# Performance work log

Measured on AMD Instinct MI355X. Metric: run time of the kernel, lower is better.

## Reference

```python
import jax, jax.numpy as jnp
import numpy as np

B, V, D = 2048, 3129, 768  # batch, answer vocab, BERT embed dim


def setup_inputs() -> dict:
    key = jax.random.key(0)
    k1, k2, k3, k4 = jax.random.split(key, 4)
    prediction = jax.random.normal(k1, (B, V), dtype=jnp.float32)
    # sparse multi-label soft scores: ~10 nonzero answers per row (VQA-style)
    soft = jax.random.uniform(k2, (B, V), dtype=jnp.float32)
    keep = jax.random.uniform(k3, (B, V)) < 0.003
    label = jnp.where(keep, soft, 0.0)
    Embedding = jax.random.normal(k4, (V, D), dtype=jnp.float32)
    return {"prediction": prediction, "label": label, "Embedding": Embedding}


def reference(prediction, label, Embedding):
    V_ = Embedding.shape[0]
    # cosine-style normalization of the Gram matrix (row norms of sim itself,
    # exactly as in the torch code)
    sim = Embedding @ Embedding.T                              # [V, V]
    n = jnp.sqrt((sim ** 2).sum(1, keepdims=True))             # [V, 1]
    sim = sim / (n @ n.T + 1e-8)
    sim = jnp.where(jnp.eye(V_, dtype=bool), -2.0, sim)        # mask diagonal
    mapping = jnp.argmax(sim, axis=1)                          # [V] int

    # vectorized replacement of the per-batch/per-nonzero python loop:
    # semantic_a[i, mapping[g]] = label[i, g] for every nonzero label[i, g].
    # entries with label==0 are routed to out-of-bounds index V and dropped.
    Bn = label.shape[0]
    idx = jnp.where(label != 0, mapping[None, :], V_)          # [B, V]
    rows = jnp.arange(Bn)[:, None]                             # [B, 1]
    semantic_a = jnp.zeros_like(label).at[rows, idx].set(label, mode="drop")

    # BCE-with-logits, mean reduction, scaled by labels.size(1)
    bce = jnp.logaddexp(0.0, prediction) - prediction * semantic_a
    return jnp.mean(bce) * V_
```

## Files before the change

kernel.cpp:

```cpp
#include <hip/hip_runtime.h>
#include <hip/hip_bf16.h>

#define VN 3129
#define DN 768
#define BN 2048
#define NT 3200
#define NB64 50
#define NTRI64 1275
#define NBLK_LOGEXP 512
#define NBLK_COMPACT 512
#define GRID_MEGA2 (NTRI64 + NBLK_LOGEXP + NBLK_COMPACT)

typedef __attribute__((ext_vector_type(8))) short bf16x8;
typedef __attribute__((ext_vector_type(4))) float f32x4;

typedef __attribute__((address_space(3))) void as3_void;
typedef __attribute__((address_space(1))) const void as1_cvoid;

__device__ __forceinline__ void gload16(const void* g, void* l) {
    __builtin_amdgcn_global_load_lds((as1_cvoid*)g, (as3_void*)l, 16, 0, 0);
}

__device__ __forceinline__ unsigned sortable_f32(float f) {
    unsigned u = __float_as_uint(f);
    return (u & 0x80000000u) ? ~u : (u | 0x80000000u);
}

__device__ __forceinline__ int xcd_swz(int orig) {
    const int q = NTRI64 / 8, r = NTRI64 % 8;
    int xcd = orig & 7, idx = orig >> 3;
    return (xcd < r ? xcd * (q + 1) : r * (q + 1) + (xcd - r) * q) + idx;
}

static const size_t WB_EB  = 0;
static const size_t WB_SIM = 4915200;
static const size_t WB_N2  = 15360000;
static const size_t WB_ARG = 15372800;
static const size_t WB_P1  = 15385600;
static const size_t WB_P2  = 15393792;
static const size_t WB_GSL = 15401984;
static const size_t WB_LSL = 15926272;
static const size_t WB_CNT = 16450560;
static const size_t WS_NEEDED = 16458752;

__global__ __launch_bounds__(256) void k_prep2(const float* __restrict__ E,
                                               unsigned short* __restrict__ Eb,
                                               unsigned* __restrict__ zwords) {
    const int gid = blockIdx.x * 256 + threadIdx.x;
    const int gstride = gridDim.x * 256;

    for (int i = gid; i < 6400; i += gstride) zwords[i] = 0u;

    const int nchunks = NT * DN / 8;
    for (int chunk = gid; chunk < nchunks; chunk += gstride) {
        int row = chunk / (DN / 8);
        int cc = (chunk % (DN / 8)) * 8;
        unsigned short o[8];
        if (row < VN) {
            const float* src = E + (size_t)row * DN + cc;
            float4 a = *(const float4*)src;
            float4 b = *(const float4*)(src + 4);
            float v[8] = {a.x, a.y, a.z, a.w, b.x, b.y, b.z, b.w};
#pragma unroll
            for (int t = 0; t < 8; ++t) {
                unsigned u = __float_as_uint(v[t]);
                u += 0x7FFFu + ((u >> 16) & 1u);
                o[t] = (unsigned short)(u >> 16);
            }
        } else {
#pragma unroll
            for (int t = 0; t < 8; ++t) o[t] = 0;
        }
        *(uint4*)(Eb + (size_t)chunk * 8) = *(const uint4*)o;
    }
}

__global__ __launch_bounds__(256) void k_gram64s(const unsigned short* __restrict__ Eb,
                                                 float* __restrict__ n2,
                                                 unsigned short* __restrict__ simT) {
    __shared__ __align__(16) unsigned short As[64 * 64];
    __shared__ __align__(16) unsigned short Bs[64 * 64];
    const int tid = threadIdx.x;
    const int lane = tid & 63;
    const int w = tid >> 6;
    const int wr = w >> 1, wc = w & 1;

    int t = xcd_swz(blockIdx.x), bi = 0, rem = t;
    while (rem >= NB64 - bi) { rem -= NB64 - bi; ++bi; }
    const int bj = bi + rem;
    const int i0 = bi * 64, j0 = bj * 64;

    const int srow = lane >> 3;
    const int scol = 8 * ((lane & 7) ^ (lane >> 3));

    f32x4 acc[2][2] = {};

    for (int k0 = 0; k0 < DN; k0 += 64) {
#pragma unroll
        for (int q = 0; q < 2; ++q) {
            int ci = w * 2 + q;
            int row = ci * 8 + srow;
            gload16(Eb + (size_t)(i0 + row) * DN + k0 + scol, As + ci * 512);
            gload16(Eb + (size_t)(j0 + row) * DN + k0 + scol, Bs + ci * 512);
        }
        __syncthreads();
        const int rA = wr * 32 + (lane & 15);
        const int rB = wc * 32 + (lane & 15);
        const int swr = (lane & 7) << 4;
        const int kb = (lane >> 4) * 16;
#pragma unroll
        for (int ks = 0; ks < 2; ++ks) {
            const int cb = (kb + ks * 64) ^ swr;
            bf16x8 af[2], bfr[2];
#pragma unroll
            for (int m = 0; m < 2; ++m)
                af[m] = *(const bf16x8*)((const char*)As + (rA + m * 16) * 128 + cb);
#pragma unroll
            for (int n = 0; n < 2; ++n)
                bfr[n] = *(const bf16x8*)((const char*)Bs + (rB + n * 16) * 128 + cb);
#pragma unroll
            for (int m = 0; m < 2; ++m)
#pragma unroll
                for (int n = 0; n < 2; ++n)
                    acc[m][n] = __builtin_amdgcn_mfma_f32_16x16x32_bf16(
                        af[m], bfr[n], acc[m][n], 0, 0, 0);
        }
        __syncthreads();
    }

    const int rr4 = (lane >> 4) * 4;

    {
        unsigned op[8];
#pragma unroll
        for (int m = 0; m < 2; ++m)
#pragma unroll
            for (int n = 0; n < 2; ++n)
#pragma unroll
                for (int ih = 0; ih < 2; ++ih) {
                    unsigned lo = __float_as_uint(acc[m][n][ih * 2]);
                    lo += 0x7FFFu + ((lo >> 16) & 1u);
                    unsigned hi = __float_as_uint(acc[m][n][ih * 2 + 1]);
                    hi += 0x7FFFu + ((hi >> 16) & 1u);
                    op[(m * 2 + n) * 2 + ih] = (lo >> 16) | (hi & 0xFFFF0000u);
                }
        uint4* dst = (uint4*)(simT + (size_t)t * 4096 + (size_t)tid * 16);
        dst[0] = *(uint4*)&op[0];
        dst[1] = *(uint4*)&op[4];
    }

    __shared__ float red[64];
    if (tid < 64) red[tid] = 0.f;
    __syncthreads();
#pragma unroll
    for (int m = 0; m < 2; ++m)
#pragma unroll
        for (int i = 0; i < 4; ++i) {
            float s = acc[m][0][i] * acc[m][0][i] + acc[m][1][i] * acc[m][1][i];
            s += __shfl_xor(s, 1); s += __shfl_xor(s, 2);
            s += __shfl_xor(s, 4); s += __shfl_xor(s, 8);
            if ((lane & 15) == 0)
                atomicAdd(&red[wr * 32 + m * 16 + rr4 + i], s);
        }
    __syncthreads();
    if (tid < 64) atomicAdd(&n2[i0 + tid], red[tid]);
    if (bi != bj) {
        __syncthreads();
        if (tid < 64) red[tid] = 0.f;
        __syncthreads();
#pragma unroll
        for (int n = 0; n < 2; ++n) {
            float s = 0.f;
#pragma unroll
            for (int m = 0; m < 2; ++m)
#pragma unroll
                for (int i = 0; i < 4; ++i) { float x = acc[m][n][i]; s += x * x; }
            s += __shfl_xor(s, 16); s += __shfl_xor(s, 32);
            if (lane < 16)
                atomicAdd(&red[wc * 32 + n * 16 + lane], s);
        }
        __syncthreads();
        if (tid < 64) atomicAdd(&n2[j0 + tid], red[tid]);
    }
}

__global__ __launch_bounds__(256) void k_mega2(const unsigned short* __restrict__ simT,
                                               const float* __restrict__ pred,
                                               const float* __restrict__ label,
                                               const float* __restrict__ n2,
                                               unsigned* __restrict__ argbest,
                                               float* __restrict__ part1,
                                               unsigned* __restrict__ gsl,
                                               float* __restrict__ lsl,
                                               unsigned* __restrict__ cntarr) {
    const int bid = blockIdx.x;
    const int tid = threadIdx.x;
    const int lane = tid & 63;
    const int w = tid >> 6;

    if (bid < NTRI64) {
        const int wr = w >> 1, wc = w & 1;
        int t = xcd_swz(bid), bi = 0, rem = t;
        while (rem >= NB64 - bi) { rem -= NB64 - bi; ++bi; }
        const int bj = bi + rem;
        const int i0 = bi * 64, j0 = bj * 64;

        __shared__ float rni_s[64], rnj_s[64];
        __shared__ unsigned rbest[64], cbest[64];
        if (tid < 64) {
            rni_s[tid] = rsqrtf(n2[i0 + tid]);
            rnj_s[tid] = rsqrtf(n2[j0 + tid]);
            rbest[tid] = 0u; cbest[tid] = 0u;
        }
        __syncthreads();

        const uint4* src = (const uint4*)(simT + (size_t)t * 4096 + (size_t)tid * 16);
        uint4 iv0 = src[0], iv1 = src[1];
        unsigned ip[8];
        *(uint4*)&ip[0] = iv0; *(uint4*)&ip[4] = iv1;

        const int rr4 = (lane >> 4) * 4;
        int rg[8]; float rni8[8];
#pragma unroll
        for (int m = 0; m < 2; ++m)
#pragma unroll
            for (int i = 0; i < 4; ++i) {
                int rl = wr * 32 + m * 16 + rr4 + i;
                rg[m * 4 + i] = i0 + rl;
                rni8[m * 4 + i] = rni_s[rl];
            }
        int cg2[2]; float rnj2[2];
#pragma unroll
        for (int n = 0; n < 2; ++n) {
            int cl = wc * 32 + n * 16 + (lane & 15);
            cg2[n] = j0 + cl;
            rnj2[n] = rnj_s[cl];
        }

#pragma unroll
        for (int m = 0; m < 2; ++m)
#pragma unroll
            for (int i = 0; i < 4; ++i) {
                int ig = rg[m * 4 + i];
                unsigned best = 0u;
#pragma unroll
                for (int n = 0; n < 2; ++n) {
                    int jg = cg2[n];
                    if (jg < VN && jg != ig) {
                        unsigned wv = ip[(m * 2 + n) * 2 + (i >> 1)];
                        float v = __uint_as_float((i & 1) ? (wv & 0xFFFF0000u) : (wv << 16));
                        unsigned key = (sortable_f32(v * rnj2[n]) & 0xFFFFF000u) | (unsigned)jg;
                        best = max(best, key);
                    }
                }
                best = max(best, __shfl_xor(best, 1));
                best = max(best, __shfl_xor(best, 2));
                best = max(best, __shfl_xor(best, 4));
                best = max(best, __shfl_xor(best, 8));
                if ((lane & 15) == 0)
                    atomicMax(&rbest[wr * 32 + m * 16 + rr4 + i], best);
            }

        if (bi != bj) {
#pragma unroll
            for (int n = 0; n < 2; ++n) {
                unsigned best = 0u;
#pragma unroll
                for (int m = 0; m < 2; ++m)
#pragma unroll
                    for (int i = 0; i < 4; ++i) {
                        int ig = rg[m * 4 + i];
                        if (ig < VN) {
                            unsigned wv = ip[(m * 2 + n) * 2 + (i >> 1)];
                            float v = __uint_as_float((i & 1) ? (wv & 0xFFFF0000u) : (wv << 16));
                            unsigned key = (sortable_f32(v * rni8[m * 4 + i]) & 0xFFFFF000u)
                                           | (unsigned)ig;
                            best = max(best, key);
                        }
                    }
                best = max(best, __shfl_xor(best, 16));
                best = max(best, __shfl_xor(best, 32));
                if (lane < 16)
                    atomicMax(&cbest[wc * 32 + n * 16 + lane], best);
            }
        }
        __syncthreads();
        if (tid < 64) {
            unsigned rb = rbest[tid];
            if (rb) atomicMax(&argbest[i0 + tid], rb);
            if (bi != bj) {
                unsigned cb = cbest[tid];
                if (cb) atomicMax(&argbest[j0 + tid], cb);
            }
        }
    } else if (bid < NTRI64 + NBLK_LOGEXP) {
        const int rb = bid - NTRI64;
        const float4* p4 = (const float4*)pred;
        const int n4 = BN * VN / 4;
        float acc = 0.f;
        for (int i = rb * 256 + tid; i < n4; i += NBLK_LOGEXP * 256) {
            float4 v = p4[i];
            acc += fmaxf(v.x, 0.f) + __logf(1.f + __expf(-fabsf(v.x)));
            acc += fmaxf(v.y, 0.f) + __logf(1.f + __expf(-fabsf(v.y)));
            acc += fmaxf(v.z, 0.f) + __logf(1.f + __expf(-fabsf(v.z)));
            acc += fmaxf(v.w, 0.f) + __logf(1.f + __expf(-fabsf(v.w)));
        }
        for (int off = 32; off; off >>= 1) acc += __shfl_down(acc, off);
        __shared__ float wsum[4];
        if (lane == 0) wsum[w] = acc;
        __syncthreads();
        if (tid == 0) part1[rb] = wsum[0] + wsum[1] + wsum[2] + wsum[3];
    } else {
        const int row = (bid - NTRI64 - NBLK_LOGEXP) * 4 + w;
        if (row < BN) {
            const float* lrow = label + (size_t)row * VN;
            float4 buf[12];
#pragma unroll
            for (int c = 0; c < 12; ++c)
                buf[c] = *(const float4*)(lrow + c * 256 + lane * 4);
            float tailv = 0.f;
            const int gtail = 3072 + lane;
            if (lane < VN - 3072) tailv = lrow[gtail];

            int base = 0;
#pragma unroll
            for (int c = 0; c < 12; ++c) {
                const float* f = (const float*)&buf[c];
#pragma unroll
                for (int e = 0; e < 4; ++e) {
                    float l = f[e];
                    unsigned long long mask = __ballot(l != 0.f);
                    if (l != 0.f) {
                        int pos = base + __popcll(mask & ((1ull << lane) - 1ull));
                        if (pos < 64) {
                            gsl[row * 64 + pos] = (unsigned)(c * 256 + lane * 4 + e);
                            lsl[row * 64 + pos] = l;
                        }
                    }
                    base += __popcll(mask);
                }
            }
            {
                unsigned long long mask = __ballot(tailv != 0.f);
                if (tailv != 0.f) {
                    int pos = base + __popcll(mask & ((1ull << lane) - 1ull));
                    if (pos < 64) {
                        gsl[row * 64 + pos] = (unsigned)gtail;
                        lsl[row * 64 + pos] = tailv;
                    }
                }
                base += __popcll(mask);
            }
            if (lane == 0) cntarr[row] = (unsigned)base;
        }
    }
}

__global__ __launch_bounds__(64) void k_scatter(const float* __restrict__ pred,
                                                const float* __restrict__ label,
                                                const unsigned* __restrict__ argbest,
                                                const unsigned* __restrict__ gsl,
                                                const float* __restrict__ lsl,
                                                const unsigned* __restrict__ cntarr,
                                                float* __restrict__ part2) {
    const int i = blockIdx.x;
    const int lane = threadIdx.x;
    const int cnt = (int)cntarr[i];
    float contrib = 0.f;

    if (cnt <= 64) {
        unsigned g = 0, tgt = 0xFFFFFFFFu;
        float l = 0.f;
        if (lane < cnt) {
            g = gsl[i * 64 + lane];
            l = lsl[i * 64 + lane];
            tgt = argbest[g] & 0xFFFu;
        }
        __shared__ unsigned tg_s[64], g_s[64];
        tg_s[lane] = tgt; g_s[lane] = g;
        __syncthreads();
        if (lane < cnt) {
            bool keep = true;
            for (int o = 0; o < cnt; ++o)
                if (tg_s[o] == tgt && g_s[o] > g) { keep = false; break; }
            if (keep) contrib = pred[(size_t)i * VN + tgt] * l;
        }
    } else {
        __shared__ int c2;
        __shared__ unsigned short gs2[256], ts2[256];
        __shared__ float ls2[256];
        if (lane == 0) c2 = 0;
        __syncthreads();
        const float* lrow = label + (size_t)i * VN;
        for (int g = lane; g < VN; g += 64) {
            float l = lrow[g];
            if (l != 0.f) {
                int p = atomicAdd(&c2, 1);
                if (p < 256) {
                    gs2[p] = (unsigned short)g;
                    ls2[p] = l;
                    ts2[p] = (unsigned short)(argbest[g] & 0xFFFu);
                }
            }
        }
        __syncthreads();
        int m = min(c2, 256);
        for (int e = lane; e < m; e += 64) {
            bool keep = true;
            for (int o = 0; o < m; ++o)
                if (ts2[o] == ts2[e] && gs2[o] > gs2[e]) keep = false;
            if (keep) contrib += pred[(size_t)i * VN + ts2[e]] * ls2[e];
        }
    }

    for (int off = 32; off; off >>= 1) contrib += __shfl_down(contrib, off);
    if (lane == 0) part2[i] = contrib;
}

__global__ __launch_bounds__(256) void k_final(const float* __restrict__ part1, int p1n,
                                               const float* __restrict__ part2,
                                               float* __restrict__ out) {
    int tid = threadIdx.x;
    double acc = 0.0;
    for (int i = tid; i < p1n; i += 256) acc += (double)part1[i];
    for (int i = tid; i < BN; i += 256) acc -= (double)part2[i];
    __shared__ double red[256];
    red[tid] = acc;
    __syncthreads();
    for (int s = 128; s; s >>= 1) {
        if (tid < s) red[tid] += red[tid + s];
        __syncthreads();
    }
    if (tid == 0) out[0] = (float)(red[0] / (double)BN);
}

__global__ __launch_bounds__(256) void k_zero(unsigned int* p, int nwords) {
    int idx = blockIdx.x * 256 + threadIdx.x;
    for (int i = idx; i < nwords; i += gridDim.x * 256) p[i] = 0u;
}

__global__ __launch_bounds__(256) void k_logexp(const float* __restrict__ pred,
                                                float* __restrict__ part1) {
    int tid = threadIdx.x;
    const float4* p4 = (const float4*)pred;
    const int n4 = BN * VN / 4;
    float acc = 0.f;
    for (int i = blockIdx.x * 256 + tid; i < n4; i += gridDim.x * 256) {
        float4 v = p4[i];
        acc += fmaxf(v.x, 0.f) + log1pf(__expf(-fabsf(v.x)));
        acc += fmaxf(v.y, 0.f) + log1pf(__expf(-fabsf(v.y)));
        acc += fmaxf(v.z, 0.f) + log1pf(__expf(-fabsf(v.z)));
        acc += fmaxf(v.w, 0.f) + log1pf(__expf(-fabsf(v.w)));
    }
    for (int off = 32; off; off >>= 1) acc += __shfl_down(acc, off);
    __shared__ float wsum[4];
    int lane = tid & 63, wid = tid >> 6;
    if (lane == 0) wsum[wid] = acc;
    __syncthreads();
    if (tid == 0) part1[blockIdx.x] = wsum[0] + wsum[1] + wsum[2] + wsum[3];
}

template <int PASS>
__global__ __launch_bounds__(256) void k_gemm(const float* __restrict__ E,
                                              float* __restrict__ n2,
                                              unsigned* __restrict__ argbest) {
    __shared__ float As[16][132];
    __shared__ float Bs[16][132];
    const int tid = threadIdx.x;
    const int tx = tid & 15, ty = tid >> 4;
    const int i0 = blockIdx.y * 128, j0 = blockIdx.x * 128;
    float acc[8][8] = {};

    for (int k0 = 0; k0 < DN; k0 += 16) {
#pragma unroll
        for (int h = 0; h < 2; ++h) {
            int f = tid + h * 256;
            int r = f >> 2;
            int kq = (f & 3) << 2;
            int gi = i0 + r;
            float4 va = make_float4(0.f, 0.f, 0.f, 0.f);
            if (gi < VN) va = *(const float4*)(E + gi * DN + k0 + kq);
            As[kq + 0][r] = va.x; As[kq + 1][r] = va.y;
            As[kq + 2][r] = va.z; As[kq + 3][r] = va.w;
            int gj = j0 + r;
            float4 vb = make_float4(0.f, 0.f, 0.f, 0.f);
            if (gj < VN) vb = *(const float4*)(E + gj * DN + k0 + kq);
            Bs[kq + 0][r] = vb.x; Bs[kq + 1][r] = vb.y;
            Bs[kq + 2][r] = vb.z; Bs[kq + 3][r] = vb.w;
        }
        __syncthreads();
#pragma unroll
        for (int k = 0; k < 16; ++k) {
            float a[8], b[8];
            *(float4*)&a[0] = *(const float4*)&As[k][ty * 8];
            *(float4*)&a[4] = *(const float4*)&As[k][ty * 8 + 4];
            *(float4*)&b[0] = *(const float4*)&Bs[k][tx * 8];
            *(float4*)&b[4] = *(const float4*)&Bs[k][tx * 8 + 4];
#pragma unroll
            for (int m = 0; m < 8; ++m)
#pragma unroll
                for (int n = 0; n < 8; ++n)
                    acc[m][n] = fmaf(a[m], b[n], acc[m][n]);
        }
        __syncthreads();
    }

    if (PASS == 0) {
        __shared__ float nrow[128];
        if (tid < 128) nrow[tid] = 0.f;
        __syncthreads();
#pragma unroll
        for (int m = 0; m < 8; ++m) {
            float s = 0.f;
#pragma unroll
            for (int n = 0; n < 8; ++n) s += acc[m][n] * acc[m][n];
            atomicAdd(&nrow[ty * 8 + m], s);
        }
        __syncthreads();
        if (tid < 128 && i0 + tid < VN) atomicAdd(&n2[i0 + tid], nrow[tid]);
    } else {
        __shared__ unsigned brow[128];
        if (tid < 128) brow[tid] = 0u;
        __syncthreads();
        float rnj[8];
#pragma unroll
        for (int n = 0; n < 8; ++n) {
            int j = j0 + tx * 8 + n;
            rnj[n] = (j < VN) ? rsqrtf(n2[j]) : 0.f;
        }
#pragma unroll
        for (int m = 0; m < 8; ++m) {
            int i = i0 + ty * 8 + m;
            unsigned best = 0u;
#pragma unroll
            for (int n = 0; n < 8; ++n) {
                int j = j0 + tx * 8 + n;
                if (j < VN && j != i) {
                    unsigned key = (sortable_f32(acc[m][n] * rnj[n]) & 0xFFFFF000u) | (unsigned)j;
                    best = max(best, key);
                }
            }
            atomicMax(&brow[ty * 8 + m], best);
        }
        __syncthreads();
        if (tid < 128 && i0 + tid < VN) atomicMax(&argbest[i0 + tid], brow[tid]);
    }
}

__global__ __launch_bounds__(256) void k_scatter_scan(const float* __restrict__ pred,
                                                      const float* __restrict__ label,
                                                      const unsigned* __restrict__ argbest,
                                                      float* __restrict__ part2) {
    int i = blockIdx.x;
    int tid = threadIdx.x;
    __shared__ int cnt;
    __shared__ unsigned short gs[256];
    __shared__ unsigned short ts[256];
    __shared__ float ls[256];
    if (tid == 0) cnt = 0;
    __syncthreads();
    const float* lrow = label + (size_t)i * VN;
    for (int g = tid; g < VN; g += 256) {
        float l = lrow[g];
        if (l != 0.f) {
            int p = atomicAdd(&cnt, 1);
            if (p < 256) {
                gs[p] = (unsigned short)g;
                ls[p] = l;
                ts[p] = (unsigned short)(argbest[g] & 0xFFFu);
            }
        }
    }
    __syncthreads();
    int m = min(cnt, 256);
    float contrib = 0.f;
    for (int e = tid; e < m; e += 256) {
        bool keep = true;
        for (int o = 0; o < m; ++o)
            if (ts[o] == ts[e] && gs[o] > gs[e]) keep = false;
        if (keep) contrib += pred[(size_t)i * VN + ts[e]] * ls[e];
    }
    for (int off = 32; off; off >>= 1) contrib += __shfl_down(contrib, off);
    __shared__ float wsum[4];
    int lane = tid & 63, wid = tid >> 6;
    if (lane == 0) wsum[wid] = contrib;
    __syncthreads();
    if (tid == 0) part2[i] = wsum[0] + wsum[1] + wsum[2] + wsum[3];
}

extern "C" void kernel_launch(void* const* d_in, const int* in_sizes, int n_in,
                              void* d_out, int out_size, void* d_ws, size_t ws_size,
                              hipStream_t stream) {
    (void)in_sizes; (void)n_in; (void)out_size;
    const float* pred  = (const float*)d_in[0];
    const float* label = (const float*)d_in[1];
    const float* E     = (const float*)d_in[2];
    float* out = (float*)d_out;
    char* wsb = (char*)d_ws;

    if (ws_size >= WS_NEEDED) {
        unsigned short* Eb   = (unsigned short*)(wsb + WB_EB);
        unsigned short* simT = (unsigned short*)(wsb + WB_SIM);
        float* n2    = (float*)(wsb + WB_N2);
        unsigned* argbest = (unsigned*)(wsb + WB_ARG);
        float* part1 = (float*)(wsb + WB_P1);
        float* part2 = (float*)(wsb + WB_P2);
        unsigned* gsl = (unsigned*)(wsb + WB_GSL);
        float* lsl   = (float*)(wsb + WB_LSL);
        unsigned* cntarr = (unsigned*)(wsb + WB_CNT);

        k_prep2<<<1024, 256, 0, stream>>>(E, Eb, (unsigned*)n2);
        k_gram64s<<<NTRI64, 256, 0, stream>>>(Eb, n2, simT);
        k_mega2<<<GRID_MEGA2, 256, 0, stream>>>(simT, pred, label, n2, argbest,
                                                part1, gsl, lsl, cntarr);
        k_scatter<<<BN, 64, 0, stream>>>(pred, label, argbest, gsl, lsl, cntarr, part2);
        k_final<<<1, 256, 0, stream>>>(part1, NBLK_LOGEXP, part2, out);
    } else {
        float* ws = (float*)d_ws;
        float* n2    = ws;
        unsigned* argbest = (unsigned*)(ws + 3200);
        float* part1 = ws + 6400;
        float* part2 = ws + 8448;
        k_zero<<<10, 256, 0, stream>>>((unsigned int*)ws, 6400);
        k_logexp<<<2048, 256, 0, stream>>>(pred, part1);
        dim3 g((VN + 127) / 128, (VN + 127) / 128);
        k_gemm<0><<<g, 256, 0, stream>>>(E, n2, argbest);
        k_gemm<1><<<g, 256, 0, stream>>>(E, n2, argbest);
        k_scatter_scan<<<BN, 256, 0, stream>>>(pred, label, argbest, part2);
        k_final<<<1, 256, 0, stream>>>(part1, 2048, part2, out);
    }
}
```

Baseline: 51.06 us.

## Compute Gram matrix with FP8 e4m3 MFMA instead of bf16

Converts the embedding table to FP8 e4m3 in the prep kernel and switches the Gram GEMM to the fp8 16x16x32 MFMA. The LDS tiles and global loads shrink to one byte per element, with a new XOR swizzle over 16-byte groups. This is meant to halve memory traffic and raise matrix throughput for the triangular Gram tiles. FP8 precision is much coarser and may flip argmax picks among near-tied similarities, which would change the mapping and the loss.

```diff
diff --git a/kernel.cpp b/kernel.cpp
--- a/kernel.cpp
+++ b/kernel.cpp
@@ -1,5 +1,6 @@
 #include <hip/hip_runtime.h>
 #include <hip/hip_bf16.h>
+#include <hip/hip_fp8.h>
 
 #define VN 3129
 #define DN 768
@@ -44,42 +45,42 @@
 static const size_t WS_NEEDED = 16458752;
 
 __global__ __launch_bounds__(256) void k_prep2(const float* __restrict__ E,
-                                               unsigned short* __restrict__ Eb,
+                                               unsigned char* __restrict__ Ef8,
                                                unsigned* __restrict__ zwords) {
     const int gid = blockIdx.x * 256 + threadIdx.x;
     const int gstride = gridDim.x * 256;
 
     for (int i = gid; i < 6400; i += gstride) zwords[i] = 0u;
 
-    const int nchunks = NT * DN / 8;
+    const int nchunks = NT * DN / 16;
     for (int chunk = gid; chunk < nchunks; chunk += gstride) {
-        int row = chunk / (DN / 8);
-        int cc = (chunk % (DN / 8)) * 8;
-        unsigned short o[8];
+        int row = chunk / (DN / 16);
+        int cc = (chunk % (DN / 16)) * 16;
+        unsigned char o[16];
         if (row < VN) {
             const float* src = E + (size_t)row * DN + cc;
-            float4 a = *(const float4*)src;
-            float4 b = *(const float4*)(src + 4);
-            float v[8] = {a.x, a.y, a.z, a.w, b.x, b.y, b.z, b.w};
-#pragma unroll
-            for (int t = 0; t < 8; ++t) {
-                unsigned u = __float_as_uint(v[t]);
-                u += 0x7FFFu + ((u >> 16) & 1u);
-                o[t] = (unsigned short)(u >> 16);
+#pragma unroll
+            for (int q = 0; q < 4; ++q) {
+                float4 v = *(const float4*)(src + q * 4);
+                __hip_fp8_e4m3 a(v.x), b(v.y), c(v.z), d(v.w);
+                o[q * 4 + 0] = a.__x;
+                o[q * 4 + 1] = b.__x;
+                o[q * 4 + 2] = c.__x;
+                o[q * 4 + 3] = d.__x;
             }
         } else {
 #pragma unroll
-            for (int t = 0; t < 8; ++t) o[t] = 0;
-        }
-        *(uint4*)(Eb + (size_t)chunk * 8) = *(const uint4*)o;
-    }
-}
-
-__global__ __launch_bounds__(256) void k_gram64s(const unsigned short* __restrict__ Eb,
+            for (int t = 0; t < 16; ++t) o[t] = 0;
+        }
+        *(uint4*)(Ef8 + (size_t)chunk * 16) = *(const uint4*)o;
+    }
+}
+
+__global__ __launch_bounds__(256) void k_gram64f(const unsigned char* __restrict__ Ef8,
                                                  float* __restrict__ n2,
                                                  unsigned short* __restrict__ simT) {
-    __shared__ __align__(16) unsigned short As[64 * 64];
-    __shared__ __align__(16) unsigned short Bs[64 * 64];
+    __shared__ __align__(16) unsigned char As[64 * 64];
+    __shared__ __align__(16) unsigned char Bs[64 * 64];
     const int tid = threadIdx.x;
     const int lane = tid & 63;
     const int w = tid >> 6;
@@ -90,40 +91,46 @@
     const int bj = bi + rem;
     const int i0 = bi * 64, j0 = bj * 64;
 
-    const int srow = lane >> 3;
-    const int scol = 8 * ((lane & 7) ^ (lane >> 3));
+    const int srow = lane >> 2;
+    const int sgr = (lane & 3) ^ (srow & 3);
+    const int scol = sgr * 16;
 
     f32x4 acc[2][2] = {};
 
     for (int k0 = 0; k0 < DN; k0 += 64) {
-#pragma unroll
-        for (int q = 0; q < 2; ++q) {
-            int ci = w * 2 + q;
-            int row = ci * 8 + srow;
-            gload16(Eb + (size_t)(i0 + row) * DN + k0 + scol, As + ci * 512);
-            gload16(Eb + (size_t)(j0 + row) * DN + k0 + scol, Bs + ci * 512);
+        {
+            int row = w * 16 + srow;
+            gload16(Ef8 + (size_t)(i0 + row) * DN + k0 + scol, As + w * 1024 + lane * 16);
+            gload16(Ef8 + (size_t)(j0 + row) * DN + k0 + scol, Bs + w * 1024 + lane * 16);
         }
         __syncthreads();
         const int rA = wr * 32 + (lane & 15);
         const int rB = wc * 32 + (lane & 15);
-        const int swr = (lane & 7) << 4;
-        const int kb = (lane >> 4) * 16;
+        const int kk = (lane >> 4) * 8;
 #pragma unroll
         for (int ks = 0; ks < 2; ++ks) {
-            const int cb = (kb + ks * 64) ^ swr;
-            bf16x8 af[2], bfr[2];
+            const int cbyte = ks * 32 + kk;
+            const int goff = cbyte & 15;
+            const int glog = cbyte >> 4;
+            long a[2], b[2];
+#pragma unroll
+            for (int m = 0; m < 2; ++m) {
+                int r = rA + m * 16;
+                int g = glog ^ (r & 3);
+                a[m] = *(const long*)(As + r * 64 + g * 16 + goff);
+            }
+#pragma unroll
+            for (int n = 0; n < 2; ++n) {
+                int r = rB + n * 16;
+                int g = glog ^ (r & 3);
+                b[n] = *(const long*)(Bs + r * 64 + g * 16 + goff);
+            }
 #pragma unroll
             for (int m = 0; m < 2; ++m)
-                af[m] = *(const bf16x8*)((const char*)As + (rA + m * 16) * 128 + cb);
-#pragma unroll
-            for (int n = 0; n < 2; ++n)
-                bfr[n] = *(const bf16x8*)((const char*)Bs + (rB + n * 16) * 128 + cb);
-#pragma unroll
-            for (int m = 0; m < 2; ++m)
 #pragma unroll
                 for (int n = 0; n < 2; ++n)
-                    acc[m][n] = __builtin_amdgcn_mfma_f32_16x16x32_bf16(
-                        af[m], bfr[n], acc[m][n], 0, 0, 0);
+                    acc[m][n] = __builtin_amdgcn_mfma_f32_16x16x32_fp8_fp8(
+                        a[m], b[n], acc[m][n], 0, 0, 0);
         }
         __syncthreads();
     }
@@ -599,7 +606,7 @@
     char* wsb = (char*)d_ws;
 
     if (ws_size >= WS_NEEDED) {
-        unsigned short* Eb   = (unsigned short*)(wsb + WB_EB);
+        unsigned char* Ef8   = (unsigned char*)(wsb + WB_EB);
         unsigned short* simT = (unsigned short*)(wsb + WB_SIM);
         float* n2    = (float*)(wsb + WB_N2);
         unsigned* argbest = (unsigned*)(wsb + WB_ARG);
@@ -609,8 +616,8 @@
         float* lsl   = (float*)(wsb + WB_LSL);
         unsigned* cntarr = (unsigned*)(wsb + WB_CNT);
 
-        k_prep2<<<1024, 256, 0, stream>>>(E, Eb, (unsigned*)n2);
-        k_gram64s<<<NTRI64, 256, 0, stream>>>(Eb, n2, simT);
+        k_prep2<<<1024, 256, 0, stream>>>(E, Ef8, (unsigned*)n2);
+        k_gram64f<<<NTRI64, 256, 0, stream>>>(Ef8, n2, simT);
         k_mega2<<<GRID_MEGA2, 256, 0, stream>>>(simT, pred, label, n2, argbest,
                                                 part1, gsl, lsl, cntarr);
         k_scatter<<<BN, 64, 0, stream>>>(pred, label, argbest, gsl, lsl, cntarr, part2);
```

New measurement: 54.08 us. 1.06x slower.
